# Optimization experiments

Measured on AMD Instinct MI355X. Metric: run time of the kernel, lower is better.

Reference implementation:

```python
import jax, jax.numpy as jnp
import numpy as np
from jax import lax

DT = 1.0  # self.dt


def setup_inputs() -> dict:
    key = jax.random.key(0)
    k1, k2 = jax.random.split(key)
    B, T, D = 16, 4096, 512
    x = jax.random.normal(k1, (B, T, D), dtype=jnp.float32)
    W = jax.random.normal(k2, (D,), dtype=jnp.float32)  # CustomLinearLayer.weight
    return {"x": x, "W": W}


def reference(x, W):
    # w = exp(-exp(W)) - 1 in (-1, 0]; w_res = sqrt(1 - w^2)
    w = jnp.exp(-jnp.exp(W)) - 1.0          # [D]
    w_res = jnp.sqrt(1.0 - w * w)           # [D]
    a = 1.0 + DT * w                        # decay factor per channel, [D]
    b = DT * w_res                          # input scale per channel, [D]

    # h_{t+1} = h_t + dt * (h_t * w + x_t * w_res) = a * h_t + b * x_t
    bx = x * b                              # [B, T, D] (fused elementwise)
    xt = jnp.swapaxes(bx, 0, 1)             # [T, B, D] scan over time

    def step(h, u):
        h_next = a * h + u
        return h_next, h_next

    h0 = jnp.zeros(x.shape[:1] + x.shape[2:], dtype=x.dtype)  # [B, D]
    _, hs = lax.scan(step, h0, xt)          # hs: [T, B, D]
    return jnp.swapaxes(hs, 0, 1)           # [B, T, D] (return_sequences=True)
```

## Files before the change

### kernel.cpp

```cpp
#include <hip/hip_runtime.h>


#define BB 16
#define TT 4096
#define DD 512
#define KK 128
#define LL (TT / KK)
#define D4 (DD / 4)

typedef float vfloat4 __attribute__((ext_vector_type(4)));

__device__ __forceinline__ void coeffs(const float* __restrict__ W, int d,
                                       float& a0, float& a1, float& a2, float& a3,
                                       float& b0, float& b1, float& b2, float& b3) {
    float e, w;
    e = expf(-expf(W[d + 0])); a0 = e; w = e - 1.0f; b0 = sqrtf(1.0f - w * w);
    e = expf(-expf(W[d + 1])); a1 = e; w = e - 1.0f; b1 = sqrtf(1.0f - w * w);
    e = expf(-expf(W[d + 2])); a2 = e; w = e - 1.0f; b2 = sqrtf(1.0f - w * w);
    e = expf(-expf(W[d + 3])); a3 = e; w = e - 1.0f; b3 = sqrtf(1.0f - w * w);
}

__global__ __launch_bounds__(256) void lru_phase1(const float4* __restrict__ x,
                                                  const float* __restrict__ W,
                                                  float4* __restrict__ E) {
    const int d4 = threadIdx.x;
    const int k  = blockIdx.x * 2 + threadIdx.y;
    const int b  = blockIdx.y;
    const int d  = d4 * 4;

    float a0, a1, a2, a3, b0, b1, b2, b3;
    coeffs(W, d, a0, a1, a2, a3, b0, b1, b2, b3);

    const float4* xp = x + ((size_t)b * TT + (size_t)k * LL) * D4 + d4;
    float h0 = 0.f, h1 = 0.f, h2 = 0.f, h3 = 0.f;
#pragma unroll 8
    for (int i = 0; i < LL; ++i) {
        float4 v = xp[(size_t)i * D4];
        h0 = a0 * h0 + b0 * v.x;
        h1 = a1 * h1 + b1 * v.y;
        h2 = a2 * h2 + b2 * v.z;
        h3 = a3 * h3 + b3 * v.w;
    }
    E[((size_t)b * KK + k) * D4 + d4] = make_float4(h0, h1, h2, h3);
}

__global__ __launch_bounds__(D4) void lru_phase2(const float* __restrict__ W,
                                                 const float4* __restrict__ E,
                                                 float4* __restrict__ C) {
    const int d4 = threadIdx.x;
    const int b  = blockIdx.x;
    const int d  = d4 * 4;

    float a0, a1, a2, a3, b0, b1, b2, b3;
    coeffs(W, d, a0, a1, a2, a3, b0, b1, b2, b3);

    float aL0 = a0, aL1 = a1, aL2 = a2, aL3 = a3;
#pragma unroll
    for (int s = 0; s < 5; ++s) { aL0 *= aL0; aL1 *= aL1; aL2 *= aL2; aL3 *= aL3; }

    float c0 = 0.f, c1 = 0.f, c2 = 0.f, c3 = 0.f;
    const size_t row = (size_t)b * KK * D4 + d4;
#pragma unroll 8
    for (int k = 0; k < KK; ++k) {
        float4 e = E[row + (size_t)k * D4];
        C[row + (size_t)k * D4] = make_float4(c0, c1, c2, c3);
        c0 = aL0 * c0 + e.x;
        c1 = aL1 * c1 + e.y;
        c2 = aL2 * c2 + e.z;
        c3 = aL3 * c3 + e.w;
    }
}

__global__ __launch_bounds__(256) void lru_phase3(const float4* __restrict__ x,
                                                  const float* __restrict__ W,
                                                  const float4* __restrict__ C,
                                                  float4* __restrict__ out) {
    const int d4 = threadIdx.x;
    const int k  = blockIdx.x * 2 + threadIdx.y;
    const int b  = blockIdx.y;
    const int d  = d4 * 4;

    float a0, a1, a2, a3, b0, b1, b2, b3;
    coeffs(W, d, a0, a1, a2, a3, b0, b1, b2, b3);

    float4 c = C[((size_t)b * KK + k) * D4 + d4];
    float h0 = c.x, h1 = c.y, h2 = c.z, h3 = c.w;

    const size_t base = ((size_t)b * TT + (size_t)k * LL) * D4 + d4;
    const float4* xp = x + base;
    vfloat4* op = (vfloat4*)(out + base);
#pragma unroll 8
    for (int i = 0; i < LL; ++i) {
        float4 v = xp[(size_t)i * D4];
        h0 = a0 * h0 + b0 * v.x;
        h1 = a1 * h1 + b1 * v.y;
        h2 = a2 * h2 + b2 * v.z;
        h3 = a3 * h3 + b3 * v.w;
        vfloat4 o; o.x = h0; o.y = h1; o.z = h2; o.w = h3;
        __builtin_nontemporal_store(o, &op[(size_t)i * D4]);
    }
}

extern "C" void kernel_launch(void* const* d_in, const int* in_sizes, int n_in,
                              void* d_out, int out_size, void* d_ws, size_t ws_size,
                              hipStream_t stream) {
    const float4* x = (const float4*)d_in[0];
    const float*  W = (const float*)d_in[1];
    float4* out = (float4*)d_out;

    char* ws = (char*)d_ws;
    float4* E = (float4*)ws;
    float4* C = (float4*)(ws + (size_t)BB * KK * DD * 4);

    dim3 grid(KK / 2, BB);
    dim3 block(D4, 2);
    lru_phase1<<<grid, block, 0, stream>>>(x, W, E);
    lru_phase2<<<dim3(BB), dim3(D4), 0, stream>>>(W, E, C);
    lru_phase3<<<grid, block, 0, stream>>>(x, W, C, out);
}
```

Baseline: 259.9 us.

## Replace three-phase chunked scan with single-pass decoupled lookback scan

Merges the three kernels (chunk reduce, carry scan, re-scan) into one kernel. Tiles get dynamic ticket IDs, publish aggregate and inclusive prefixes with flags, and do a decoupled lookback to find their carry. Each thread keeps its 32 input rows in registers, so x is read from global memory once instead of twice. In exchange it adds spin-wait synchronization, an extra memset, and heavy register pressure from holding 32 float4 values per thread.

```diff
diff --git a/kernel.cpp b/kernel.cpp
--- a/kernel.cpp
+++ b/kernel.cpp
@@ -4,117 +4,119 @@
 #define BB 16
 #define TT 4096
 #define DD 512
-#define KK 128
-#define LL (TT / KK)
 #define D4 (DD / 4)
+#define HL 32
+#define SL 64
+#define NS (TT / SL)
+#define NSC (BB * NS)
 
 typedef float vfloat4 __attribute__((ext_vector_type(4)));
 
-__device__ __forceinline__ void coeffs(const float* __restrict__ W, int d,
-                                       float& a0, float& a1, float& a2, float& a3,
-                                       float& b0, float& b1, float& b2, float& b3) {
-    float e, w;
-    e = expf(-expf(W[d + 0])); a0 = e; w = e - 1.0f; b0 = sqrtf(1.0f - w * w);
-    e = expf(-expf(W[d + 1])); a1 = e; w = e - 1.0f; b1 = sqrtf(1.0f - w * w);
-    e = expf(-expf(W[d + 2])); a2 = e; w = e - 1.0f; b2 = sqrtf(1.0f - w * w);
-    e = expf(-expf(W[d + 3])); a3 = e; w = e - 1.0f; b3 = sqrtf(1.0f - w * w);
-}
+#define SCOPE_AGENT __HIP_MEMORY_SCOPE_AGENT
 
-__global__ __launch_bounds__(256) void lru_phase1(const float4* __restrict__ x,
-                                                  const float* __restrict__ W,
-                                                  float4* __restrict__ E) {
+__global__ __launch_bounds__(256, 2) void lru_lookback(
+    const vfloat4* __restrict__ x, const float* __restrict__ W,
+    vfloat4* __restrict__ out,
+    int* __restrict__ flags, int* __restrict__ ticket,
+    vfloat4* __restrict__ Agg, vfloat4* __restrict__ Inc)
+{
+    __shared__ vfloat4 sE0[D4];
+    __shared__ int s_tile;
+
     const int d4 = threadIdx.x;
-    const int k  = blockIdx.x * 2 + threadIdx.y;
-    const int b  = blockIdx.y;
-    const int d  = d4 * 4;
+    const int ty = threadIdx.y;
 
-    float a0, a1, a2, a3, b0, b1, b2, b3;
-    coeffs(W, d, a0, a1, a2, a3, b0, b1, b2, b3);
+    if (threadIdx.x == 0 && ty == 0) s_tile = atomicAdd(ticket, 1);
+    __syncthreads();
+    const int tile = s_tile;
+    const int b = tile & (BB - 1);
+    const int s = tile >> 4;
 
-    const float4* xp = x + ((size_t)b * TT + (size_t)k * LL) * D4 + d4;
-    float h0 = 0.f, h1 = 0.f, h2 = 0.f, h3 = 0.f;
-#pragma unroll 8
-    for (int i = 0; i < LL; ++i) {
-        float4 v = xp[(size_t)i * D4];
-        h0 = a0 * h0 + b0 * v.x;
-        h1 = a1 * h1 + b1 * v.y;
-        h2 = a2 * h2 + b2 * v.z;
-        h3 = a3 * h3 + b3 * v.w;
+    const vfloat4 wv = ((const vfloat4*)W)[d4];
+    vfloat4 a;
+    a.x = expf(-expf(wv.x)); a.y = expf(-expf(wv.y));
+    a.z = expf(-expf(wv.z)); a.w = expf(-expf(wv.w));
+    const vfloat4 w1 = a - 1.0f;
+    vfloat4 bs;
+    bs.x = sqrtf(1.0f - w1.x * w1.x); bs.y = sqrtf(1.0f - w1.y * w1.y);
+    bs.z = sqrtf(1.0f - w1.z * w1.z); bs.w = sqrtf(1.0f - w1.w * w1.w);
+    vfloat4 a32 = a;
+#pragma unroll
+    for (int i = 0; i < 5; ++i) a32 *= a32;
+    const vfloat4 a64 = a32 * a32;
+
+    const size_t rowbase = ((size_t)b * TT + (size_t)s * SL + (size_t)ty * HL) * D4 + d4;
+    const vfloat4* xp = x + rowbase;
+    vfloat4 xr[HL];
+    vfloat4 h = {0.f, 0.f, 0.f, 0.f};
+#pragma unroll
+    for (int i = 0; i < HL; ++i) {
+        vfloat4 v = __builtin_nontemporal_load(&xp[(size_t)i * D4]);
+        xr[i] = v;
+        h = a * h + bs * v;
     }
-    E[((size_t)b * KK + k) * D4 + d4] = make_float4(h0, h1, h2, h3);
-}
 
-__global__ __launch_bounds__(D4) void lru_phase2(const float* __restrict__ W,
-                                                 const float4* __restrict__ E,
-                                                 float4* __restrict__ C) {
-    const int d4 = threadIdx.x;
-    const int b  = blockIdx.x;
-    const int d  = d4 * 4;
+    if (ty == 0) sE0[d4] = h;
+    __syncthreads();
 
-    float a0, a1, a2, a3, b0, b1, b2, b3;
-    coeffs(W, d, a0, a1, a2, a3, b0, b1, b2, b3);
+    const size_t vi = (size_t)tile * D4 + d4;
+    vfloat4 agg = {0.f, 0.f, 0.f, 0.f};
+    if (ty == 1) {
+        agg = h + a32 * sE0[d4];
+        Agg[vi] = agg;
+    }
+    __syncthreads();
+    if (threadIdx.x == 0 && ty == 0)
+        __hip_atomic_store(&flags[tile], 1, __ATOMIC_RELEASE, SCOPE_AGENT);
 
-    float aL0 = a0, aL1 = a1, aL2 = a2, aL3 = a3;
+    vfloat4 c = {0.f, 0.f, 0.f, 0.f};
+    vfloat4 m = {1.f, 1.f, 1.f, 1.f};
+    int j = s - 1;
+    while (j >= 0) {
+        const int fj = j * BB + b;
+        int st = __hip_atomic_load(&flags[fj], __ATOMIC_RELAXED, SCOPE_AGENT);
+        while (st == 0) {
+            __builtin_amdgcn_s_sleep(1);
+            st = __hip_atomic_load(&flags[fj], __ATOMIC_RELAXED, SCOPE_AGENT);
+        }
+        __builtin_amdgcn_fence(__ATOMIC_ACQUIRE, "agent");
+        const vfloat4 v = (st == 2) ? Inc[(size_t)fj * D4 + d4]
+                                    : Agg[(size_t)fj * D4 + d4];
+        c = c + m * v;
+        if (st == 2) break;
+        m = m * a64;
+        --j;
+    }
+
+    if (ty == 1) Inc[vi] = agg + a64 * c;
+    __syncthreads();
+    if (threadIdx.x == 0 && ty == 0)
+        __hip_atomic_store(&flags[tile], 2, __ATOMIC_RELEASE, SCOPE_AGENT);
+
+    vfloat4 g = (ty == 0) ? c : (sE0[d4] + a32 * c);
+    vfloat4* op = out + rowbase;
 #pragma unroll
-    for (int s = 0; s < 5; ++s) { aL0 *= aL0; aL1 *= aL1; aL2 *= aL2; aL3 *= aL3; }
-
-    float c0 = 0.f, c1 = 0.f, c2 = 0.f, c3 = 0.f;
-    const size_t row = (size_t)b * KK * D4 + d4;
-#pragma unroll 8
-    for (int k = 0; k < KK; ++k) {
-        float4 e = E[row + (size_t)k * D4];
-        C[row + (size_t)k * D4] = make_float4(c0, c1, c2, c3);
-        c0 = aL0 * c0 + e.x;
-        c1 = aL1 * c1 + e.y;
-        c2 = aL2 * c2 + e.z;
-        c3 = aL3 * c3 + e.w;
-    }
-}
-
-__global__ __launch_bounds__(256) void lru_phase3(const float4* __restrict__ x,
-                                                  const float* __restrict__ W,
-                                                  const float4* __restrict__ C,
-                                                  float4* __restrict__ out) {
-    const int d4 = threadIdx.x;
-    const int k  = blockIdx.x * 2 + threadIdx.y;
-    const int b  = blockIdx.y;
-    const int d  = d4 * 4;
-
-    float a0, a1, a2, a3, b0, b1, b2, b3;
-    coeffs(W, d, a0, a1, a2, a3, b0, b1, b2, b3);
-
-    float4 c = C[((size_t)b * KK + k) * D4 + d4];
-    float h0 = c.x, h1 = c.y, h2 = c.z, h3 = c.w;
-
-    const size_t base = ((size_t)b * TT + (size_t)k * LL) * D4 + d4;
-    const float4* xp = x + base;
-    vfloat4* op = (vfloat4*)(out + base);
-#pragma unroll 8
-    for (int i = 0; i < LL; ++i) {
-        float4 v = xp[(size_t)i * D4];
-        h0 = a0 * h0 + b0 * v.x;
-        h1 = a1 * h1 + b1 * v.y;
-        h2 = a2 * h2 + b2 * v.z;
-        h3 = a3 * h3 + b3 * v.w;
-        vfloat4 o; o.x = h0; o.y = h1; o.z = h2; o.w = h3;
-        __builtin_nontemporal_store(o, &op[(size_t)i * D4]);
+    for (int i = 0; i < HL; ++i) {
+        g = a * g + bs * xr[i];
+        __builtin_nontemporal_store(g, &op[(size_t)i * D4]);
     }
 }
 
 extern "C" void kernel_launch(void* const* d_in, const int* in_sizes, int n_in,
                               void* d_out, int out_size, void* d_ws, size_t ws_size,
                               hipStream_t stream) {
-    const float4* x = (const float4*)d_in[0];
-    const float*  W = (const float*)d_in[1];
-    float4* out = (float4*)d_out;
+    const vfloat4* x = (const vfloat4*)d_in[0];
+    const float*   W = (const float*)d_in[1];
+    vfloat4* out = (vfloat4*)d_out;
 
     char* ws = (char*)d_ws;
-    float4* E = (float4*)ws;
-    float4* C = (float4*)(ws + (size_t)BB * KK * DD * 4);
+    int*     flags  = (int*)ws;
+    int*     ticket = (int*)(ws + 4096);
+    vfloat4* Agg    = (vfloat4*)(ws + 65536);
+    vfloat4* Inc    = (vfloat4*)(ws + 65536 + (size_t)NSC * DD * 4);
 
-    dim3 grid(KK / 2, BB);
-    dim3 block(D4, 2);
-    lru_phase1<<<grid, block, 0, stream>>>(x, W, E);
-    lru_phase2<<<dim3(BB), dim3(D4), 0, stream>>>(W, E, C);
-    lru_phase3<<<grid, block, 0, stream>>>(x, W, C, out);
+    hipMemsetAsync(ws, 0, 8192, stream);
+
+    lru_lookback<<<dim3(NSC), dim3(D4, 2), 0, stream>>>(x, W, out, flags, ticket,
+                                                        Agg, Inc);
 }
```

Measured after the change: 480.1 us. 1.85x slower.
